# Performance work log

Measured on AMD Instinct MI355X. Metric: run time of the kernel, lower is better.

The kernel has to match this reference:

```python
import jax, jax.numpy as jnp
import numpy as np
from jax import lax

NF = 64
RED = 16  # CALayer / CBAM channel reduction


def conv1x1(x, w, b):
    # x: [B,Ci,H,W], w: [Co,Ci], b: [Co]
    return jnp.einsum('oi,bihw->bohw', w, x) + b[None, :, None, None]


def calayer(x, w1, b1, w2, b2):
    # SE-style channel attention (RCAN CALayer): global avg pool -> 1x1 conv -> ReLU -> 1x1 conv -> sigmoid
    y = x.mean(axis=(2, 3))                      # [B,C]
    z = jax.nn.relu(y @ w1.T + b1)               # [B,C//RED]
    s = jax.nn.sigmoid(z @ w2.T + b2)            # [B,C]
    return x * s[:, :, None, None]


def mean_variance_norm(x, eps=1e-5):
    # per-sample, per-channel spatial instance norm (AdaAttN style)
    m = x.mean(axis=(2, 3), keepdims=True)
    v = x.var(axis=(2, 3), keepdims=True)
    return (x - m) / jnp.sqrt(v + eps)


def cbam(x, mlp_w1, mlp_b1, mlp_w2, mlp_b2, sp_w, sp_b):
    # BasicAttentionBlockv1 assumed to be a CBAM block (docstring: "CBAM")
    avg = x.mean(axis=(2, 3))                    # [B,C]
    mx = x.max(axis=(2, 3))                      # [B,C]
    def mlp(v):
        return jax.nn.relu(v @ mlp_w1.T + mlp_b1) @ mlp_w2.T + mlp_b2
    s = jax.nn.sigmoid(mlp(avg) + mlp(mx))       # [B,C]
    x = x * s[:, :, None, None]
    sp_in = jnp.concatenate([x.mean(axis=1, keepdims=True), x.max(axis=1, keepdims=True)], axis=1)  # [B,2,H,W]
    m = lax.conv_general_dilated(sp_in, sp_w, (1, 1), 'SAME',
                                 dimension_numbers=('NCHW', 'OIHW', 'NCHW')) + sp_b[None, :, None, None]
    return x * jax.nn.sigmoid(m)


def setup_inputs() -> dict:
    key = jax.random.key(0)
    ks = iter(jax.random.split(key, 64))
    B, N, C, H, W = 4, 3, NF, 64, 64
    r = lambda shape, s=0.05: jax.random.normal(next(ks), shape, dtype=jnp.float32) * s
    inp = {
        'group': jax.random.normal(next(ks), (B, N, C, H, W), dtype=jnp.float32),
        'FG': jax.random.normal(next(ks), (B, N, C, H, W), dtype=jnp.float32),
        'BG': jax.random.normal(next(ks), (B, N, C, H, W), dtype=jnp.float32),
        # conv_group_1 (3nf->3nf 1x1), CALayer(3nf), conv_group_2 (3nf->nf), conv_group_3 (nf->nf)
        'wg1': r((3 * C, 3 * C)), 'bg1': r((3 * C,)),
        'cag_w1': r((3 * C // RED, 3 * C)), 'cag_b1': r((3 * C // RED,)),
        'cag_w2': r((3 * C, 3 * C // RED)), 'cag_b2': r((3 * C,)),
        'wg2': r((C, 3 * C)), 'bg2': r((C,)),
        'wg3': r((C, C)), 'bg3': r((C,)),
        # conv_center_1, CALayer(nf), conv_center_2
        'wc1': r((C, C)), 'bc1': r((C,)),
        'cac_w1': r((C // RED, C)), 'cac_b1': r((C // RED,)),
        'cac_w2': r((C, C // RED)), 'cac_b2': r((C,)),
        'wc2': r((C, C)), 'bc2': r((C,)),
        # f, g, h 1x1 convs
        'f_w': r((C, C)), 'f_b': r((C,)),
        'g_w': r((C, C)), 'g_b': r((C,)),
        'h_w': r((C, C)), 'h_b': r((C,)),
        # CBAM params
        'mlp_w1': r((C // RED, C)), 'mlp_b1': r((C // RED,)),
        'mlp_w2': r((C, C // RED)), 'mlp_b2': r((C,)),
        'sp_w': r((1, 2, 7, 7)), 'sp_b': r((1,)),
    }
    return inp


def reference(group, FG, BG,
              wg1, bg1, cag_w1, cag_b1, cag_w2, cag_b2, wg2, bg2, wg3, bg3,
              wc1, bc1, cac_w1, cac_b1, cac_w2, cac_b2, wc2, bc2,
              f_w, f_b, g_w, g_b, h_w, h_b,
              mlp_w1, mlp_b1, mlp_w2, mlp_b2, sp_w, sp_b):
    B, N, C, H, W = group.shape
    center = group[:, 1]
    FGc = FG[:, 1]
    BGc = BG[:, 1]
    grp = group.reshape(B, N * C, H, W)

    fea_group = conv1x1(grp, wg1, bg1)
    fea_group = calayer(fea_group, cag_w1, cag_b1, cag_w2, cag_b2)
    fea_group = conv1x1(fea_group, wg2, bg2)
    fea_group = conv1x1(fea_group, wg3, bg3)

    fea_center = conv1x1(center, wc1, bc1)
    fea_center = calayer(fea_center, cac_w1, cac_b1, cac_w2, cac_b2)
    fea_center = conv1x1(fea_center, wc2, bc2)

    Fq = conv1x1(fea_group, f_w, f_b).reshape(B, C, H * W).transpose(0, 2, 1)   # [B,HW,C]
    Gk = conv1x1(fea_center, g_w, g_b).reshape(B, C, H * W)                     # [B,C,HW]
    Hv = conv1x1(BGc, h_w, h_b).reshape(B, C, H * W).transpose(0, 2, 1)         # [B,HW,C]

    S = jax.nn.softmax(jnp.einsum('bqc,bck->bqk', Fq, Gk), axis=-1)             # [B,HW,HW]
    mean = jnp.einsum('bqk,bkc->bqc', S, Hv)                                    # [B,HW,C]
    second = jnp.einsum('bqk,bkc->bqc', S, Hv * Hv)
    std = jnp.sqrt(jax.nn.relu(second - mean * mean))

    mean = mean.reshape(B, H, W, C).transpose(0, 3, 1, 2)
    std = std.reshape(B, H, W, C).transpose(0, 3, 1, 2)

    transfer_FG = std * mean_variance_norm(FGc) + mean
    out = cbam(transfer_FG + BGc, mlp_w1, mlp_b1, mlp_w2, mlp_b2, sp_w, sp_b)
    return out
```

## Files before the change

kernel.cpp:

```cpp
#include <hip/hip_runtime.h>
#include <hip/hip_bf16.h>
#include <math.h>

#define HW 4096

typedef __attribute__((ext_vector_type(8))) short bf16x8;
typedef __attribute__((ext_vector_type(4))) float f32x4;

static __device__ __forceinline__ unsigned short f2bf(float x) {
    unsigned u = __float_as_uint(x);
    u += 0x7fffu + ((u >> 16) & 1u);
    return (unsigned short)(u >> 16);
}
static __device__ __forceinline__ float bf2f(unsigned short h) {
    return __uint_as_float((unsigned)h << 16);
}
static __device__ __forceinline__ float g4(const float4& v, int k) {
    return k == 0 ? v.x : k == 1 ? v.y : k == 2 ? v.z : v.w;
}

__global__ __launch_bounds__(256) void k_transpose2(
    const float* __restrict__ group, const float* __restrict__ BGc, int bstride,
    unsigned short* __restrict__ X0T, unsigned short* __restrict__ BGcT)
{
    extern __shared__ float lds[];
    const int b = blockIdx.y, p0 = blockIdx.x << 6, t = threadIdx.x;
    const int z = blockIdx.z;
    const int C = z ? 64 : 192;
    const float* xb = (z ? BGc : group) + (size_t)b * bstride;
    unsigned short* outT = z ? BGcT : X0T;
    for (int idx = t; idx < (C << 6); idx += 256) {
        int c = idx >> 6, p = idx & 63;
        lds[c * 65 + p] = xb[(size_t)c * HW + p0 + p];
    }
    __syncthreads();
    unsigned short* ob = outT + ((size_t)b * HW + p0) * C;
    for (int idx = t; idx < (C << 6); idx += 256) {
        int p = idx / C, c = idx - p * C;
        ob[idx] = f2bf(lds[c * 65 + p]);
    }
}

__global__ __launch_bounds__(256) void k_xmean(
    const float* __restrict__ g, int bstride, float* __restrict__ xmean)
{
    int bc = blockIdx.x;
    int b = bc / 192, ci = bc - b * 192;
    const float* p = g + (size_t)b * bstride + (size_t)ci * HW;
    int t = threadIdx.x;
    float s = 0.f;
    #pragma unroll 4
    for (int i = t; i < HW; i += 256) s += p[i];
    for (int o = 32; o > 0; o >>= 1) s += __shfl_down(s, o, 64);
    __shared__ float red[4];
    if ((t & 63) == 0) red[t >> 6] = s;
    __syncthreads();
    if (t == 0) xmean[bc] = (red[0] + red[1] + red[2] + red[3]) * (1.0f / HW);
}

static __device__ __forceinline__ void gemm64_tile(
    const float* A, const float* B, int t, float acc[4][4])
{
    const int tr = t >> 4, tc = t & 15;
    #pragma unroll
    for (int i = 0; i < 4; ++i)
        #pragma unroll
        for (int j = 0; j < 4; ++j) acc[i][j] = 0.f;
    for (int k4 = 0; k4 < 64; k4 += 4) {
        float4 a[4], bb[4];
        #pragma unroll
        for (int i = 0; i < 4; ++i) a[i]  = *(const float4*)&A[(4 * tr + i) * 68 + k4];
        #pragma unroll
        for (int kk = 0; kk < 4; ++kk) bb[kk] = *(const float4*)&B[(k4 + kk) * 68 + 4 * tc];
        #pragma unroll
        for (int i = 0; i < 4; ++i)
            #pragma unroll
            for (int kk = 0; kk < 4; ++kk)
                #pragma unroll
                for (int j = 0; j < 4; ++j)
                    acc[i][j] = fmaf(g4(a[i], kk), g4(bb[kk], j), acc[i][j]);
    }
}

__global__ __launch_bounds__(256) void k_prep(
    const float* __restrict__ xmean,
    const float* __restrict__ wg1, const float* __restrict__ bg1,
    const float* __restrict__ cag_w1, const float* __restrict__ cag_b1,
    const float* __restrict__ cag_w2, const float* __restrict__ cag_b2,
    const float* __restrict__ wc1, const float* __restrict__ bc1,
    const float* __restrict__ cac_w1, const float* __restrict__ cac_b1,
    const float* __restrict__ cac_w2, const float* __restrict__ cac_b2,
    const float* __restrict__ wg2, const float* __restrict__ bg2,
    const float* __restrict__ wg3, const float* __restrict__ bg3,
    const float* __restrict__ wc2, const float* __restrict__ bc2,
    const float* __restrict__ wf, const float* __restrict__ fb,
    const float* __restrict__ wgw, const float* __restrict__ gbv,
    const float* __restrict__ wh,
    float* __restrict__ W3L, float* __restrict__ Uf,
    float* __restrict__ bQ0L, float* __restrict__ bK0,
    float* __restrict__ sgG, float* __restrict__ scG,
    unsigned short* __restrict__ whb, unsigned short* __restrict__ wg1b)
{
    const float LOG2E = 1.4426950408889634f;
    __shared__ float sA[64 * 68], sB[64 * 68], sC[64 * 68];
    __shared__ float xm[192], pg[192], pc[64], zz[16];
    const int bid = blockIdx.x, t = threadIdx.x;

    if (bid >= 4) {
        const int x = bid - 4;
        #pragma unroll
        for (int j = 0; j < 16; ++j) {
            int idx = t + j * 256, r = idx >> 6, c = idx & 63;
            sA[r * 68 + c] = wf[idx];
            sB[r * 68 + c] = wg3[idx];
        }
        __syncthreads();
        float acc[4][4];
        gemm64_tile(sA, sB, t, acc);
        {
            const int tr = t >> 4, tc = t & 15;
            #pragma unroll
            for (int i = 0; i < 4; ++i)
                #pragma unroll
                for (int j = 0; j < 4; ++j)
                    sC[(4 * tr + i) * 68 + 4 * tc + j] = acc[i][j];
        }
        __syncthreads();
        if (x == 0 && t < 64) {
            float a = fb[t];
            #pragma unroll 16
            for (int m = 0; m < 64; ++m) {
                a = fmaf(sC[t * 68 + m], bg2[m], a);
                a = fmaf(sA[t * 68 + m], bg3[m], a);
            }
            bQ0L[t] = a * LOG2E;
        }
        __syncthreads();
        for (int idx = t; idx < 3072; idx += 256) {
            int c = idx >> 6, m = idx & 63;
            sA[c * 68 + m] = wg2[m * 192 + x * 48 + c];
        }
        __syncthreads();
        {
            const int tr = t >> 4, tc = t & 15;
            float a2[4][3];
            #pragma unroll
            for (int i = 0; i < 4; ++i)
                #pragma unroll
                for (int j = 0; j < 3; ++j) a2[i][j] = 0.f;
            for (int k4 = 0; k4 < 64; k4 += 4) {
                float4 a[4], bb[3];
                #pragma unroll
                for (int i = 0; i < 4; ++i) a[i] = *(const float4*)&sC[(4 * tr + i) * 68 + k4];
                #pragma unroll
                for (int j = 0; j < 3; ++j) bb[j] = *(const float4*)&sA[(3 * tc + j) * 68 + k4];
                #pragma unroll
                for (int i = 0; i < 4; ++i)
                    #pragma unroll
                    for (int j = 0; j < 3; ++j)
                        #pragma unroll
                        for (int kk = 0; kk < 4; ++kk)
                            a2[i][j] = fmaf(g4(a[i], kk), g4(bb[j], kk), a2[i][j]);
            }
            #pragma unroll
            for (int i = 0; i < 4; ++i)
                #pragma unroll
                for (int j = 0; j < 3; ++j)
                    W3L[(4 * tr + i) * 192 + x * 48 + 3 * tc + j] = a2[i][j] * LOG2E;
        }
        if (x == 1) {
            __syncthreads();
            #pragma unroll
            for (int j = 0; j < 16; ++j) {
                int idx = t + j * 256, r = idx >> 6, c = idx & 63;
                sA[r * 68 + c] = wgw[idx];
                sB[r * 68 + c] = wc2[idx];
            }
            __syncthreads();
            float au[4][4];
            gemm64_tile(sA, sB, t, au);
            {
                const int tr = t >> 4, tc = t & 15;
                #pragma unroll
                for (int i = 0; i < 4; ++i)
                    #pragma unroll
                    for (int j = 0; j < 4; ++j)
                        Uf[(4 * tr + i) * 64 + 4 * tc + j] = au[i][j];
            }
            if (t < 64) {
                float a = gbv[t];
                #pragma unroll 16
                for (int m = 0; m < 64; ++m) a = fmaf(sA[t * 68 + m], bc2[m], a);
                bK0[t] = a;
            }
        }
        for (int idx = t; idx < 9216; idx += 256) {
            int g = x * 9216 + idx;
            wg1b[g] = f2bf(wg1[g]);
        }
        return;
    }

    const int b = bid, w = t >> 6, lane = t & 63;
    if (t < 192) xm[t] = xmean[b * 192 + t];
    __syncthreads();
    for (int r = w; r < 192; r += 4) {
        float part = 0.f;
        #pragma unroll
        for (int j = 0; j < 3; ++j)
            part = fmaf(wg1[r * 192 + lane + 64 * j], xm[lane + 64 * j], part);
        #pragma unroll
        for (int o = 32; o > 0; o >>= 1) part += __shfl_down(part, o, 64);
        if (lane == 0) pg[r] = part + bg1[r];
    }
    for (int r = w; r < 64; r += 4) {
        float part = wc1[r * 64 + lane] * xm[64 + lane];
        #pragma unroll
        for (int o = 32; o > 0; o >>= 1) part += __shfl_down(part, o, 64);
        if (lane == 0) pc[r] = part + bc1[r];
    }
    __syncthreads();
    if (t < 12) {
        float a = cag_b1[t];
        #pragma unroll 16
        for (int i = 0; i < 192; ++i) a = fmaf(cag_w1[t * 192 + i], pg[i], a);
        zz[t] = fmaxf(a, 0.f);
    }
    if (t >= 64 && t < 68) {
        int r = t - 64;
        float a = cac_b1[r];
        #pragma unroll 16
        for (int i = 0; i < 64; ++i) a = fmaf(cac_w1[r * 64 + i], pc[i], a);
        zz[12 + r] = fmaxf(a, 0.f);
    }
    __syncthreads();
    if (t < 192) {
        float a = cag_b2[t];
        #pragma unroll
        for (int j = 0; j < 12; ++j) a = fmaf(cag_w2[t * 12 + j], zz[j], a);
        sgG[b * 192 + t] = 1.f / (1.f + __expf(-a));
    } else {
        int c = t - 192;
        float a = cac_b2[c];
        #pragma unroll
        for (int j = 0; j < 4; ++j) a = fmaf(cac_w2[c * 4 + j], zz[12 + j], a);
        scG[b * 64 + c] = 1.f / (1.f + __expf(-a));
    }
    if (b == 0) {
        #pragma unroll
        for (int j = 0; j < 16; ++j) whb[t + j * 256] = f2bf(wh[t + j * 256]);
    }
}

__global__ __launch_bounds__(256) void k_wscale(
    const float* __restrict__ W3L, const float* __restrict__ Uf,
    const float* __restrict__ sgG, const float* __restrict__ scG,
    const float* __restrict__ wc1, const float* __restrict__ bc1,
    const float* __restrict__ bK0,
    unsigned short* __restrict__ WQs, unsigned short* __restrict__ WKb,
    float* __restrict__ biasK)
{
    const int bid = blockIdx.x, t = threadIdx.x;
    if (bid < 192) {
        int i = bid * 256 + t;
        int b = i / 12288, rem = i - b * 12288;
        int c = rem % 192;
        WQs[i] = f2bf(W3L[rem] * sgG[b * 192 + c]);
        return;
    }
    __shared__ float Usc[64 * 68], sW[64 * 68], u2[64];
    const int b = bid - 192;
    #pragma unroll
    for (int j = 0; j < 16; ++j) {
        int idx = t + j * 256, r = idx >> 6, c = idx & 63;
        Usc[r * 68 + c] = Uf[idx] * scG[b * 64 + c];
        sW[r * 68 + c]  = wc1[idx];
    }
    if (t < 64) u2[t] = scG[b * 64 + t] * bc1[t];
    __syncthreads();
    float acc[4][4];
    gemm64_tile(Usc, sW, t, acc);
    const int tr = t >> 4, tc = t & 15;
    #pragma unroll
    for (int i = 0; i < 4; ++i)
        #pragma unroll
        for (int j = 0; j < 4; ++j)
            WKb[(size_t)b * 4096 + (4 * tr + i) * 64 + 4 * tc + j] = f2bf(acc[i][j]);
    if (t < 64) {
        float a = bK0[t];
        #pragma unroll 16
        for (int m = 0; m < 64; ++m) a = fmaf(Uf[t * 64 + m], u2[m], a);
        biasK[b * 64 + t] = a;
    }
}

__global__ __launch_bounds__(256) void k_gconv(
    const unsigned short* __restrict__ X0T, const unsigned short* __restrict__ wg1b,
    const float* __restrict__ bg1, unsigned short* __restrict__ g1T)
{
    const int t = threadIdx.x;
    const int w = t >> 6, lane = t & 63;
    const int gid = lane >> 4, cid = lane & 15;
    const int b = blockIdx.z;
    const int p0 = blockIdx.x << 6;
    const int co16 = ((blockIdx.y << 2) + w) << 4;
    const unsigned short* xrow = X0T + (size_t)b * HW * 192;
    const unsigned short* wr = wg1b + (size_t)co16 * 192;
    f32x4 acc[4];
    #pragma unroll
    for (int n = 0; n < 4; ++n)
        #pragma unroll
        for (int r = 0; r < 4; ++r)
            acc[n][r] = bg1[co16 + 4 * gid + r];
    for (int kc = 0; kc < 192; kc += 32) {
        bf16x8 a = *(const bf16x8*)(wr + (size_t)cid * 192 + kc + 8 * gid);
        #pragma unroll
        for (int n = 0; n < 4; ++n) {
            bf16x8 bfr = *(const bf16x8*)(xrow + (size_t)(p0 + 16 * n + cid) * 192 + kc + 8 * gid);
            acc[n] = __builtin_amdgcn_mfma_f32_16x16x32_bf16(a, bfr, acc[n], 0, 0, 0);
        }
    }
    #pragma unroll
    for (int n = 0; n < 4; ++n)
        #pragma unroll
        for (int r = 0; r < 4; ++r)
            g1T[((size_t)b * HW + p0 + 16 * n + cid) * 192 + co16 + 4 * gid + r] = f2bf(acc[n][r]);
}

__global__ __launch_bounds__(256) void k_proj(
    const unsigned short* __restrict__ g1T, const unsigned short* __restrict__ X0T,
    const unsigned short* __restrict__ BGcT,
    const unsigned short* __restrict__ WQs, const float* __restrict__ bQ0L,
    const unsigned short* __restrict__ WKb, const float* __restrict__ biasK,
    const unsigned short* __restrict__ whb, const float* __restrict__ h_b,
    unsigned short* __restrict__ FqT, unsigned short* __restrict__ GkT,
    unsigned short* __restrict__ hvN)
{
    const int t = threadIdx.x;
    const int w = t >> 6, lane = t & 63;
    const int gid = lane >> 4, cid = lane & 15;
    const int which = blockIdx.y;
    const int b = blockIdx.z;
    const int p0 = blockIdx.x << 6;
    const int co16 = w << 4;
    int Cin, kOff, ldx;
    const unsigned short *XT, *W;
    const float* bp;
    if (which == 0)      { XT = g1T;  ldx = 192; kOff = 0;  Cin = 192; W = WQs + (size_t)b * 12288; bp = bQ0L; }
    else if (which == 1) { XT = X0T;  ldx = 192; kOff = 64; Cin = 64;  W = WKb + (size_t)b * 4096;  bp = biasK + b * 64; }
    else                 { XT = BGcT; ldx = 64;  kOff = 0;  Cin = 64;  W = whb;                      bp = h_b; }
    const unsigned short* xrow = XT + (size_t)b * HW * ldx + kOff;
    const unsigned short* wr = W + (size_t)co16 * Cin;
    f32x4 acc[4];
    #pragma unroll
    for (int n = 0; n < 4; ++n)
        #pragma unroll
        for (int r = 0; r < 4; ++r)
            acc[n][r] = bp[co16 + 4 * gid + r];
    for (int kc = 0; kc < Cin; kc += 32) {
        bf16x8 a = *(const bf16x8*)(wr + (size_t)cid * Cin + kc + 8 * gid);
        #pragma unroll
        for (int n = 0; n < 4; ++n) {
            bf16x8 bfr = *(const bf16x8*)(xrow + (size_t)(p0 + 16 * n + cid) * ldx + kc + 8 * gid);
            acc[n] = __builtin_amdgcn_mfma_f32_16x16x32_bf16(a, bfr, acc[n], 0, 0, 0);
        }
    }
    #pragma unroll
    for (int n = 0; n < 4; ++n)
        #pragma unroll
        for (int r = 0; r < 4; ++r) {
            float v = acc[n][r];
            int co = co16 + 4 * gid + r;
            int p  = p0 + 16 * n + cid;
            if (which == 0)      FqT[((size_t)b * HW + p) * 64 + co] = f2bf(v);
            else if (which == 1) GkT[((size_t)b * HW + p) * 64 + co] = f2bf(v);
            else                 hvN[((size_t)b * 64 + co) * HW + p] = f2bf(v);
        }
}

__global__ __launch_bounds__(512, 2) void k_attn(
    const unsigned short* __restrict__ FqT, const unsigned short* __restrict__ GkT,
    const unsigned short* __restrict__ HvN,
    float* __restrict__ mb, float* __restrict__ sbuf)
{
    __shared__ __align__(16) char smem[65536];
    const int t = threadIdx.x;
    const int bid = blockIdx.x;
    const int b = (bid & 7) >> 1;
    const int qbase = (((bid >> 3) << 1) | (bid & 1)) << 6;
    const int w = t >> 6, lane = t & 63;
    const int gid = lane >> 4, cid = lane & 15;
    const size_t CQ = (size_t)HW * 64;
    const unsigned short* fqt = FqT + (size_t)b * CQ;
    const unsigned short* gkt = GkT + (size_t)b * CQ;
    const unsigned short* hv  = HvN + (size_t)b * CQ;
    unsigned short* Pw = (unsigned short*)smem + w * 4096;

    bf16x8 fqa[4][2];
    #pragma unroll
    for (int qt = 0; qt < 4; ++qt) {
        const unsigned short* fr = fqt + (size_t)(qbase + 16 * qt + cid) * 64 + 8 * gid;
        fqa[qt][0] = *(const bf16x8*)fr;
        fqa[qt][1] = *(const bf16x8*)(fr + 32);
    }
    bf16x8 ones;
    #pragma unroll
    for (int j = 0; j < 8; ++j) ones[j] = (short)0x3F80;

    const f32x4 fz = {0.f, 0.f, 0.f, 0.f};
    f32x4 am[4][4], a2[4][4], lac[4];
    #pragma unroll
    for (int qt = 0; qt < 4; ++qt) {
        lac[qt] = fz;
        #pragma unroll
        for (int n = 0; n < 4; ++n) { am[qt][n] = fz; a2[qt][n] = fz; }
    }

    const int k00 = w << 9;
    for (int it = 0; it < 8; ++it) {
        const int k0 = k00 + (it << 6);
        #pragma unroll
        for (int n = 0; n < 4; ++n) {
            const unsigned short* gr = gkt + (size_t)(k0 + 16 * n + cid) * 64 + 8 * gid;
            bf16x8 b0 = *(const bf16x8*)gr;
            bf16x8 b1 = *(const bf16x8*)(gr + 32);
            const int k = 16 * n + cid;
            #pragma unroll
            for (int qt = 0; qt < 4; ++qt) {
                f32x4 s = __builtin_amdgcn_mfma_f32_16x16x32_bf16(fqa[qt][0], b0, fz, 0, 0, 0);
                s = __builtin_amdgcn_mfma_f32_16x16x32_bf16(fqa[qt][1], b1, s, 0, 0, 0);
                #pragma unroll
                for (int r = 0; r < 4; ++r) {
                    int q = 4 * gid + r;
                    Pw[qt * 1024 + q * 64 + (((k >> 3) ^ (q & 7)) << 3) + (k & 7)] =
                        f2bf(__builtin_amdgcn_exp2f(s[r]));
                }
            }
        }
        bf16x8 pa[4][2];
        #pragma unroll
        for (int qt = 0; qt < 4; ++qt)
            #pragma unroll
            for (int kh = 0; kh < 2; ++kh)
                pa[qt][kh] = *(const bf16x8*)(Pw + qt * 1024 + cid * 64 +
                                              (((4 * kh + gid) ^ (cid & 7)) << 3));
        #pragma unroll
        for (int qt = 0; qt < 4; ++qt) {
            lac[qt] = __builtin_amdgcn_mfma_f32_16x16x32_bf16(pa[qt][0], ones, lac[qt], 0, 0, 0);
            lac[qt] = __builtin_amdgcn_mfma_f32_16x16x32_bf16(pa[qt][1], ones, lac[qt], 0, 0, 0);
        }
        #pragma unroll
        for (int n = 0; n < 4; ++n) {
            const unsigned short* hr = hv + (size_t)(16 * n + cid) * HW + k0;
            #pragma unroll
            for (int kh = 0; kh < 2; ++kh) {
                bf16x8 hb = *(const bf16x8*)(hr + 32 * kh + 8 * gid);
                bf16x8 h2;
                #pragma unroll
                for (int j = 0; j < 8; ++j) {
                    float v = bf2f((unsigned short)hb[j]);
                    h2[j] = (short)f2bf(v * v);
                }
                #pragma unroll
                for (int qt = 0; qt < 4; ++qt) {
                    am[qt][n] = __builtin_amdgcn_mfma_f32_16x16x32_bf16(pa[qt][kh], hb, am[qt][n], 0, 0, 0);
                    a2[qt][n] = __builtin_amdgcn_mfma_f32_16x16x32_bf16(pa[qt][kh], h2, a2[qt][n], 0, 0, 0);
                }
            }
        }
    }

    __syncthreads();
    float* lb = (float*)smem;
    #pragma unroll
    for (int qt = 0; qt < 4; ++qt)
        *(f32x4*)(lb + ((size_t)(w * 4 + qt) * 64 + lane) * 4) = lac[qt];
    __syncthreads();
    float* Lm = (float*)(smem + 32768);
    if (t < 256) {
        int qt = t >> 6, ls = t & 63;
        f32x4 s = fz;
        #pragma unroll
        for (int ww = 0; ww < 8; ++ww)
            s += *(const f32x4*)(lb + ((size_t)(ww * 4 + qt) * 64 + ls) * 4);
        *(f32x4*)(Lm + ((size_t)qt * 64 + ls) * 4) = s;
    }
    __syncthreads();
    float* ab = (float*)smem;
    f32x4 meanv = fz;
    for (int qt = 0; qt < 4; ++qt) {
        #pragma unroll
        for (int n = 0; n < 4; ++n)
            *(f32x4*)(ab + ((size_t)(w * 4 + n) * 64 + lane) * 4) = am[qt][n];
        __syncthreads();
        if (t < 256) {
            int n = t >> 6, ls = t & 63;
            f32x4 s = fz;
            #pragma unroll
            for (int ww = 0; ww < 8; ++ww)
                s += *(const f32x4*)(ab + ((size_t)(ww * 4 + n) * 64 + ls) * 4);
            f32x4 lv = *(const f32x4*)(Lm + ((size_t)qt * 64 + ls) * 4);
            #pragma unroll
            for (int r = 0; r < 4; ++r) meanv[r] = s[r] / lv[r];
            int q0s = qbase + 16 * qt + 4 * (ls >> 4);
            int c   = 16 * n + (ls & 15);
            *(f32x4*)(mb + (size_t)b * CQ + (size_t)c * HW + q0s) = meanv;
        }
        __syncthreads();
        #pragma unroll
        for (int n = 0; n < 4; ++n)
            *(f32x4*)(ab + ((size_t)(w * 4 + n) * 64 + lane) * 4) = a2[qt][n];
        __syncthreads();
        if (t < 256) {
            int n = t >> 6, ls = t & 63;
            f32x4 s = fz;
            #pragma unroll
            for (int ww = 0; ww < 8; ++ww)
                s += *(const f32x4*)(ab + ((size_t)(ww * 4 + n) * 64 + ls) * 4);
            f32x4 lv = *(const f32x4*)(Lm + ((size_t)qt * 64 + ls) * 4);
            f32x4 sv;
            #pragma unroll
            for (int r = 0; r < 4; ++r) {
                float sec = s[r] / lv[r];
                sv[r] = sqrtf(fmaxf(sec - meanv[r] * meanv[r], 0.f));
            }
            int q0s = qbase + 16 * qt + 4 * (ls >> 4);
            int c   = 16 * n + (ls & 15);
            *(f32x4*)(sbuf + (size_t)b * CQ + (size_t)c * HW + q0s) = sv;
        }
        __syncthreads();
    }
}

__global__ __launch_bounds__(256) void k_transfer_f(
    const float* __restrict__ mb, const float* __restrict__ sb,
    const float* __restrict__ FG, const float* __restrict__ BG, int bstride,
    float* __restrict__ xb, float* __restrict__ pavg, float* __restrict__ pmaxb)
{
    __shared__ float fgl[4096];
    __shared__ float r1[4], r2[4];
    const int bc = blockIdx.x, t = threadIdx.x;
    const int b = bc >> 6, c = bc & 63;
    const size_t row = (size_t)bc * HW;
    const float* fg = FG + (size_t)b * bstride + (size_t)(64 + c) * HW;
    const float* bg = BG + (size_t)b * bstride + (size_t)(64 + c) * HW;
    float s = 0.f, s2 = 0.f;
    #pragma unroll
    for (int j = 0; j < 16; ++j) {
        int i = t + j * 256;
        float v = fg[i];
        fgl[i] = v;
        s += v; s2 += v * v;
    }
    #pragma unroll
    for (int o = 32; o > 0; o >>= 1) { s += __shfl_down(s, o, 64); s2 += __shfl_down(s2, o, 64); }
    if ((t & 63) == 0) { r1[t >> 6] = s; r2[t >> 6] = s2; }
    __syncthreads();
    float m  = (r1[0] + r1[1] + r1[2] + r1[3]) * (1.0f / HW);
    float e2 = (r2[0] + r2[1] + r2[2] + r2[3]) * (1.0f / HW);
    float rs = rsqrtf(fmaxf(e2 - m * m, 0.f) + 1e-5f);
    float psum = 0.f, pmax = -1e30f;
    #pragma unroll
    for (int j = 0; j < 16; ++j) {
        int q = t + j * 256;
        float xv = sb[row + q] * (fgl[q] - m) * rs + mb[row + q] + bg[q];
        xb[row + q] = xv;
        psum += xv; pmax = fmaxf(pmax, xv);
    }
    __syncthreads();
    #pragma unroll
    for (int o = 32; o > 0; o >>= 1) {
        psum += __shfl_down(psum, o, 64);
        pmax = fmaxf(pmax, __shfl_down(pmax, o, 64));
    }
    if ((t & 63) == 0) { r1[t >> 6] = psum; r2[t >> 6] = pmax; }
    __syncthreads();
    if (t == 0) {
        pavg[bc]  = (r1[0] + r1[1] + r1[2] + r1[3]) * (1.0f / HW);
        pmaxb[bc] = fmaxf(fmaxf(r2[0], r2[1]), fmaxf(r2[2], r2[3]));
    }
}

static __device__ __forceinline__ void cbam_scale(
    const float* __restrict__ pav, const float* __restrict__ pmx,
    const float* __restrict__ w1, const float* __restrict__ b1,
    const float* __restrict__ w2, const float* __restrict__ b2,
    int b, int t, float* scb)
{
    __shared__ float za[4], zm[4];
    if (t < 4) {
        float aa = b1[t], am = b1[t];
        #pragma unroll 16
        for (int i = 0; i < 64; ++i) {
            aa = fmaf(w1[t * 64 + i], pav[b * 64 + i], aa);
            am = fmaf(w1[t * 64 + i], pmx[b * 64 + i], am);
        }
        za[t] = fmaxf(aa, 0.f);
        zm[t] = fmaxf(am, 0.f);
    }
    __syncthreads();
    if (t < 64) {
        float a = 2.f * b2[t];
        #pragma unroll
        for (int j = 0; j < 4; ++j) a = fmaf(w2[t * 4 + j], za[j] + zm[j], a);
        scb[t] = 1.f / (1.f + __expf(-a));
    }
    __syncthreads();
}

__global__ __launch_bounds__(256) void k_sp_pool(
    const float* __restrict__ xb,
    const float* __restrict__ pav, const float* __restrict__ pmx,
    const float* __restrict__ w1, const float* __restrict__ b1,
    const float* __restrict__ w2, const float* __restrict__ b2,
    float* __restrict__ spm, float* __restrict__ spx)
{
    __shared__ float scb[64];
    const int b = blockIdx.y, t = threadIdx.x;
    cbam_scale(pav, pmx, w1, b1, w2, b2, b, t, scb);
    const int p = blockIdx.x * 256 + t;
    const float* xp = xb + (size_t)b * 262144 + p;
    float sum = 0.f, mx = -1e30f;
    #pragma unroll 8
    for (int c = 0; c < 64; ++c) {
        float v = xp[(size_t)c * HW] * scb[c];
        sum += v;
        mx = fmaxf(mx, v);
    }
    spm[b * HW + p] = sum * (1.0f / 64.0f);
    spx[b * HW + p] = mx;
}

__global__ __launch_bounds__(256) void k_spf(
    const float* __restrict__ spm, const float* __restrict__ spx,
    const float* __restrict__ w, const float* __restrict__ bias,
    const float* __restrict__ xb,
    const float* __restrict__ pav, const float* __restrict__ pmx,
    const float* __restrict__ w1, const float* __restrict__ b1,
    const float* __restrict__ w2, const float* __restrict__ b2,
    float* __restrict__ out)
{
    __shared__ float scb[64];
    const int b = blockIdx.y, t = threadIdx.x;
    cbam_scale(pav, pmx, w1, b1, w2, b2, b, t, scb);
    const int p = blockIdx.x * 256 + t;
    const int y = p >> 6, x = p & 63;
    float acc = bias[0];
    for (int dy = 0; dy < 7; ++dy) {
        int yy = y + dy - 3;
        if (yy < 0 || yy >= 64) continue;
        for (int dx = 0; dx < 7; ++dx) {
            int xx = x + dx - 3;
            if (xx < 0 || xx >= 64) continue;
            int q = b * HW + yy * 64 + xx;
            acc = fmaf(spm[q], w[dy * 7 + dx],      acc);
            acc = fmaf(spx[q], w[49 + dy * 7 + dx], acc);
        }
    }
    float sgm = 1.f / (1.f + __expf(-acc));
    const float* xp = xb + (size_t)b * 262144 + p;
    float* op = out + (size_t)b * 262144 + p;
    #pragma unroll 8
    for (int c = 0; c < 64; ++c)
        op[(size_t)c * HW] = xp[(size_t)c * HW] * scb[c] * sgm;
}

extern "C" void kernel_launch(void* const* d_in, const int* in_sizes, int n_in,
                              void* d_out, int out_size, void* d_ws, size_t ws_size,
                              hipStream_t stream)
{
    const float* group  = (const float*)d_in[0];
    const float* FG     = (const float*)d_in[1];
    const float* BG     = (const float*)d_in[2];
    const float* wg1    = (const float*)d_in[3];
    const float* bg1    = (const float*)d_in[4];
    const float* cag_w1 = (const float*)d_in[5];
    const float* cag_b1 = (const float*)d_in[6];
    const float* cag_w2 = (const float*)d_in[7];
    const float* cag_b2 = (const float*)d_in[8];
    const float* wg2    = (const float*)d_in[9];
    const float* bg2    = (const float*)d_in[10];
    const float* wg3    = (const float*)d_in[11];
    const float* bg3    = (const float*)d_in[12];
    const float* wc1    = (const float*)d_in[13];
    const float* bc1    = (const float*)d_in[14];
    const float* cac_w1 = (const float*)d_in[15];
    const float* cac_b1 = (const float*)d_in[16];
    const float* cac_w2 = (const float*)d_in[17];
    const float* cac_b2 = (const float*)d_in[18];
    const float* wc2    = (const float*)d_in[19];
    const float* bc2    = (const float*)d_in[20];
    const float* f_w    = (const float*)d_in[21];
    const float* f_b    = (const float*)d_in[22];
    const float* g_w    = (const float*)d_in[23];
    const float* g_b    = (const float*)d_in[24];
    const float* h_w    = (const float*)d_in[25];
    const float* h_b    = (const float*)d_in[26];
    const float* mlp_w1 = (const float*)d_in[27];
    const float* mlp_b1 = (const float*)d_in[28];
    const float* mlp_w2 = (const float*)d_in[29];
    const float* mlp_b2 = (const float*)d_in[30];
    const float* sp_w   = (const float*)d_in[31];
    const float* sp_b   = (const float*)d_in[32];
    float* out = (float*)d_out;

    const int B = 4;
    const size_t CHW = (size_t)64 * HW;
    const int BST = (int)(3 * CHW);

    float* ws = (float*)d_ws;
    const size_t M = 1048576;
    unsigned short* X0T  = (unsigned short*)ws;
    unsigned short* BGcT = (unsigned short*)(ws + 3 * M / 2);
    unsigned short* g1T  = (unsigned short*)(ws + 2 * M);
    unsigned short* FqT  = (unsigned short*)(ws + 7 * M / 2);
    unsigned short* GkT  = (unsigned short*)(ws + 4 * M);
    unsigned short* hvN  = (unsigned short*)(ws + 9 * M / 2);
    float* mbuf = ws + 5 * M;
    float* sbuf = ws + 6 * M;
    float* xb   = ws;
    float* smalls = ws + 7 * M;
    float* xmean = smalls;
    float* sgG   = smalls + 768;
    float* scG   = smalls + 1536;
    float* pav   = smalls + 1792;
    float* pmx   = smalls + 2048;
    float* biasK = smalls + 2304;
    float* bQ0L  = smalls + 2560;
    float* bK0   = smalls + 2624;
    float* Uf    = smalls + 2688;
    float* W3L   = smalls + 6784;
    float* spm   = smalls + 19072;
    float* spx   = smalls + 35456;
    unsigned short* wsh = (unsigned short*)(smalls + 51840);
    unsigned short* WQs  = wsh;
    unsigned short* WKb  = wsh + 49152;
    unsigned short* whb  = wsh + 65536;
    unsigned short* wg1b = wsh + 69632;

    dim3 blk(256);

    k_transpose2<<<dim3(64, B, 2), blk, 192 * 65 * 4, stream>>>(group, BG + CHW, BST, X0T, BGcT);
    k_xmean<<<B * 192, blk, 0, stream>>>(group, BST, xmean);
    k_prep<<<8, blk, 0, stream>>>(
        xmean, wg1, bg1, cag_w1, cag_b1, cag_w2, cag_b2,
        wc1, bc1, cac_w1, cac_b1, cac_w2, cac_b2,
        wg2, bg2, wg3, bg3, wc2, bc2,
        f_w, f_b, g_w, g_b, h_w,
        W3L, Uf, bQ0L, bK0, sgG, scG, whb, wg1b);
    k_wscale<<<196, blk, 0, stream>>>(W3L, Uf, sgG, scG, wc1, bc1, bK0, WQs, WKb, biasK);
    k_gconv<<<dim3(64, 3, B), blk, 0, stream>>>(X0T, wg1b, bg1, g1T);
    k_proj<<<dim3(64, 3, B), blk, 0, stream>>>(
        g1T, X0T, BGcT, WQs, bQ0L, WKb, biasK, whb, h_b, FqT, GkT, hvN);
    k_attn<<<256, 512, 0, stream>>>(FqT, GkT, hvN, mbuf, sbuf);
    k_transfer_f<<<B * 64, blk, 0, stream>>>(mbuf, sbuf, FG, BG, BST, xb, pav, pmx);
    k_sp_pool<<<dim3(HW / 256, B), blk, 0, stream>>>(xb, pav, pmx, mlp_w1, mlp_b1, mlp_w2, mlp_b2, spm, spx);
    k_spf<<<dim3(HW / 256, B), blk, 0, stream>>>(spm, spx, sp_w, sp_b, xb, pav, pmx, mlp_w1, mlp_b1, mlp_w2, mlp_b2, out);
}
```

Measured before the change: 164.5 us.

## Fuse xmean into transpose, precompute Hv squared, use packed bf16 convert

Folds the per-channel mean of the group input into the transpose kernel via wave reductions and atomics, so the separate xmean pass that re-read the input is gone (a memset is added instead). Hv*Hv is computed once in the projection kernel and stored as its own bf16 tensor, so the attention kernel no longer squares and rounds it in every block. That costs an extra global read stream in attention. Exp results are converted with the packed v_cvt_pk_bf16_f32 instruction instead of manual rounding. The workspace layout is rearranged to fit the new buffer.

Measured after the change: 203.8 us. +23.9%, slower.

```diff
diff --git a/kernel.cpp b/kernel.cpp
--- a/kernel.cpp
+++ b/kernel.cpp
@@ -12,8 +12,10 @@
     u += 0x7fffu + ((u >> 16) & 1u);
     return (unsigned short)(u >> 16);
 }
-static __device__ __forceinline__ float bf2f(unsigned short h) {
-    return __uint_as_float((unsigned)h << 16);
+static __device__ __forceinline__ unsigned cvtpk(float a, float b) {
+    unsigned d;
+    asm("v_cvt_pk_bf16_f32 %0, %1, %2" : "=v"(d) : "v"(a), "v"(b));
+    return d;
 }
 static __device__ __forceinline__ float g4(const float4& v, int k) {
     return k == 0 ? v.x : k == 1 ? v.y : k == 2 ? v.z : v.w;
@@ -21,7 +23,8 @@
 
 __global__ __launch_bounds__(256) void k_transpose2(
     const float* __restrict__ group, const float* __restrict__ BGc, int bstride,
-    unsigned short* __restrict__ X0T, unsigned short* __restrict__ BGcT)
+    unsigned short* __restrict__ X0T, unsigned short* __restrict__ BGcT,
+    float* __restrict__ xmean)
 {
     extern __shared__ float lds[];
     const int b = blockIdx.y, p0 = blockIdx.x << 6, t = threadIdx.x;
@@ -39,23 +42,15 @@
         int p = idx / C, c = idx - p * C;
         ob[idx] = f2bf(lds[c * 65 + p]);
     }
-}
-
-__global__ __launch_bounds__(256) void k_xmean(
-    const float* __restrict__ g, int bstride, float* __restrict__ xmean)
-{
-    int bc = blockIdx.x;
-    int b = bc / 192, ci = bc - b * 192;
-    const float* p = g + (size_t)b * bstride + (size_t)ci * HW;
-    int t = threadIdx.x;
-    float s = 0.f;
-    #pragma unroll 4
-    for (int i = t; i < HW; i += 256) s += p[i];
-    for (int o = 32; o > 0; o >>= 1) s += __shfl_down(s, o, 64);
-    __shared__ float red[4];
-    if ((t & 63) == 0) red[t >> 6] = s;
-    __syncthreads();
-    if (t == 0) xmean[bc] = (red[0] + red[1] + red[2] + red[3]) * (1.0f / HW);
+    if (z == 0) {
+        const int w = t >> 6, lane = t & 63;
+        for (int c = w; c < 192; c += 4) {
+            float v = lds[c * 65 + lane];
+            #pragma unroll
+            for (int o = 32; o > 0; o >>= 1) v += __shfl_down(v, o, 64);
+            if (lane == 0) atomicAdd(&xmean[b * 192 + c], v * (1.0f / HW));
+        }
+    }
 }
 
 static __device__ __forceinline__ void gemm64_tile(
@@ -334,7 +329,7 @@
     const unsigned short* __restrict__ WKb, const float* __restrict__ biasK,
     const unsigned short* __restrict__ whb, const float* __restrict__ h_b,
     unsigned short* __restrict__ FqT, unsigned short* __restrict__ GkT,
-    unsigned short* __restrict__ hvN)
+    unsigned short* __restrict__ hvN, unsigned short* __restrict__ hv2N)
 {
     const int t = threadIdx.x;
     const int w = t >> 6, lane = t & 63;
@@ -374,13 +369,17 @@
             int p  = p0 + 16 * n + cid;
             if (which == 0)      FqT[((size_t)b * HW + p) * 64 + co] = f2bf(v);
             else if (which == 1) GkT[((size_t)b * HW + p) * 64 + co] = f2bf(v);
-            else                 hvN[((size_t)b * 64 + co) * HW + p] = f2bf(v);
+            else {
+                size_t o = ((size_t)b * 64 + co) * HW + p;
+                hvN[o]  = f2bf(v);
+                hv2N[o] = f2bf(v * v);
+            }
         }
 }
 
 __global__ __launch_bounds__(512, 2) void k_attn(
     const unsigned short* __restrict__ FqT, const unsigned short* __restrict__ GkT,
-    const unsigned short* __restrict__ HvN,
+    const unsigned short* __restrict__ HvN, const unsigned short* __restrict__ Hv2N,
     float* __restrict__ mb, float* __restrict__ sbuf)
 {
     __shared__ __align__(16) char smem[65536];
@@ -394,6 +393,7 @@
     const unsigned short* fqt = FqT + (size_t)b * CQ;
     const unsigned short* gkt = GkT + (size_t)b * CQ;
     const unsigned short* hv  = HvN + (size_t)b * CQ;
+    const unsigned short* hv2 = Hv2N + (size_t)b * CQ;
     unsigned short* Pw = (unsigned short*)smem + w * 4096;
 
     bf16x8 fqa[4][2];
@@ -429,11 +429,15 @@
             for (int qt = 0; qt < 4; ++qt) {
                 f32x4 s = __builtin_amdgcn_mfma_f32_16x16x32_bf16(fqa[qt][0], b0, fz, 0, 0, 0);
                 s = __builtin_amdgcn_mfma_f32_16x16x32_bf16(fqa[qt][1], b1, s, 0, 0, 0);
+                unsigned d0 = cvtpk(__builtin_amdgcn_exp2f(s[0]), __builtin_amdgcn_exp2f(s[1]));
+                unsigned d1 = cvtpk(__builtin_amdgcn_exp2f(s[2]), __builtin_amdgcn_exp2f(s[3]));
+                unsigned short pv[4] = {
+                    (unsigned short)d0, (unsigned short)(d0 >> 16),
+                    (unsigned short)d1, (unsigned short)(d1 >> 16) };
                 #pragma unroll
                 for (int r = 0; r < 4; ++r) {
                     int q = 4 * gid + r;
-                    Pw[qt * 1024 + q * 64 + (((k >> 3) ^ (q & 7)) << 3) + (k & 7)] =
-                        f2bf(__builtin_amdgcn_exp2f(s[r]));
+                    Pw[qt * 1024 + q * 64 + (((k >> 3) ^ (q & 7)) << 3) + (k & 7)] = pv[r];
                 }
             }
         }
@@ -451,16 +455,12 @@
         }
         #pragma unroll
         for (int n = 0; n < 4; ++n) {
-            const unsigned short* hr = hv + (size_t)(16 * n + cid) * HW + k0;
+            const unsigned short* hr  = hv  + (size_t)(16 * n + cid) * HW + k0;
+            const unsigned short* hr2 = hv2 + (size_t)(16 * n + cid) * HW + k0;
             #pragma unroll
             for (int kh = 0; kh < 2; ++kh) {
-                bf16x8 hb = *(const bf16x8*)(hr + 32 * kh + 8 * gid);
-                bf16x8 h2;
-                #pragma unroll
-                for (int j = 0; j < 8; ++j) {
-                    float v = bf2f((unsigned short)hb[j]);
-                    h2[j] = (short)f2bf(v * v);
-                }
+                bf16x8 hb = *(const bf16x8*)(hr  + 32 * kh + 8 * gid);
+                bf16x8 h2 = *(const bf16x8*)(hr2 + 32 * kh + 8 * gid);
                 #pragma unroll
                 for (int qt = 0; qt < 4; ++qt) {
                     am[qt][n] = __builtin_amdgcn_mfma_f32_16x16x32_bf16(pa[qt][kh], hb, am[qt][n], 0, 0, 0);
@@ -716,10 +716,11 @@
     unsigned short* FqT  = (unsigned short*)(ws + 7 * M / 2);
     unsigned short* GkT  = (unsigned short*)(ws + 4 * M);
     unsigned short* hvN  = (unsigned short*)(ws + 9 * M / 2);
-    float* mbuf = ws + 5 * M;
-    float* sbuf = ws + 6 * M;
+    unsigned short* hv2N = (unsigned short*)(ws + 5 * M);
+    float* mbuf = ws + 2 * M;
+    float* sbuf = ws + 11 * M / 2;
     float* xb   = ws;
-    float* smalls = ws + 7 * M;
+    float* smalls = ws + 13 * M / 2;
     float* xmean = smalls;
     float* sgG   = smalls + 768;
     float* scG   = smalls + 1536;
@@ -740,8 +741,8 @@
 
     dim3 blk(256);
 
-    k_transpose2<<<dim3(64, B, 2), blk, 192 * 65 * 4, stream>>>(group, BG + CHW, BST, X0T, BGcT);
-    k_xmean<<<B * 192, blk, 0, stream>>>(group, BST, xmean);
+    hipMemsetAsync(xmean, 0, 768 * sizeof(float), stream);
+    k_transpose2<<<dim3(64, B, 2), blk, 192 * 65 * 4, stream>>>(group, BG + CHW, BST, X0T, BGcT, xmean);
     k_prep<<<8, blk, 0, stream>>>(
         xmean, wg1, bg1, cag_w1, cag_b1, cag_w2, cag_b2,
         wc1, bc1, cac_w1, cac_b1, cac_w2, cac_b2,
@@ -751,8 +752,8 @@
     k_wscale<<<196, blk, 0, stream>>>(W3L, Uf, sgG, scG, wc1, bc1, bK0, WQs, WKb, biasK);
     k_gconv<<<dim3(64, 3, B), blk, 0, stream>>>(X0T, wg1b, bg1, g1T);
     k_proj<<<dim3(64, 3, B), blk, 0, stream>>>(
-        g1T, X0T, BGcT, WQs, bQ0L, WKb, biasK, whb, h_b, FqT, GkT, hvN);
-    k_attn<<<256, 512, 0, stream>>>(FqT, GkT, hvN, mbuf, sbuf);
+        g1T, X0T, BGcT, WQs, bQ0L, WKb, biasK, whb, h_b, FqT, GkT, hvN, hv2N);
+    k_attn<<<256, 512, 0, stream>>>(FqT, GkT, hvN, hv2N, mbuf, sbuf);
     k_transfer_f<<<B * 64, blk, 0, stream>>>(mbuf, sbuf, FG, BG, BST, xb, pav, pmx);
     k_sp_pool<<<dim3(HW / 256, B), blk, 0, stream>>>(xb, pav, pmx, mlp_w1, mlp_b1, mlp_w2, mlp_b2, spm, spx);
     k_spf<<<dim3(HW / 256, B), blk, 0, stream>>>(spm, spx, sp_w, sp_b, xb, pav, pmx, mlp_w1, mlp_b1, mlp_w2, mlp_b2, out);
```

## Fold group conv1x1 into query weights and fuse channel mean into transpose

Applied to the files above, without the earlier changes.

The per-pixel 192x192 group convolution (k_gconv) is replaced by precomputing a combined per-batch weight WQF = WQs·wg1 plus a folded bias in a tiny MFMA kernel, so k_proj reads X0T directly and the g1T intermediate buffer is no longer written and re-read. The separate k_xmean pass over the group tensor is removed; k_transpose2 now writes per-tile channel partial sums from LDS and k_prep reduces them. This saves one full-resolution GEMM, its memory traffic and a kernel launch. In exchange, rounding the composed weight to bf16 changes numerics slightly, and the partial-sum buffer enlarges workspace usage.

New measurement: 170.4 us. +3.6%, slower.

```diff
diff --git a/kernel.cpp b/kernel.cpp
--- a/kernel.cpp
+++ b/kernel.cpp
@@ -21,7 +21,8 @@
 
 __global__ __launch_bounds__(256) void k_transpose2(
     const float* __restrict__ group, const float* __restrict__ BGc, int bstride,
-    unsigned short* __restrict__ X0T, unsigned short* __restrict__ BGcT)
+    unsigned short* __restrict__ X0T, unsigned short* __restrict__ BGcT,
+    float* __restrict__ xpart)
 {
     extern __shared__ float lds[];
     const int b = blockIdx.y, p0 = blockIdx.x << 6, t = threadIdx.x;
@@ -39,23 +40,16 @@
         int p = idx / C, c = idx - p * C;
         ob[idx] = f2bf(lds[c * 65 + p]);
     }
-}
-
-__global__ __launch_bounds__(256) void k_xmean(
-    const float* __restrict__ g, int bstride, float* __restrict__ xmean)
-{
-    int bc = blockIdx.x;
-    int b = bc / 192, ci = bc - b * 192;
-    const float* p = g + (size_t)b * bstride + (size_t)ci * HW;
-    int t = threadIdx.x;
-    float s = 0.f;
-    #pragma unroll 4
-    for (int i = t; i < HW; i += 256) s += p[i];
-    for (int o = 32; o > 0; o >>= 1) s += __shfl_down(s, o, 64);
-    __shared__ float red[4];
-    if ((t & 63) == 0) red[t >> 6] = s;
-    __syncthreads();
-    if (t == 0) xmean[bc] = (red[0] + red[1] + red[2] + red[3]) * (1.0f / HW);
+    if (z == 0) {
+        const int w = t >> 6, lane = t & 63;
+        float* xp = xpart + ((size_t)b * 64 + blockIdx.x) * 192;
+        for (int c = w; c < 192; c += 4) {
+            float v = lds[c * 65 + lane];
+            #pragma unroll
+            for (int o = 32; o > 0; o >>= 1) v += __shfl_down(v, o, 64);
+            if (lane == 0) xp[c] = v;
+        }
+    }
 }
 
 static __device__ __forceinline__ void gemm64_tile(
@@ -83,7 +77,7 @@
 }
 
 __global__ __launch_bounds__(256) void k_prep(
-    const float* __restrict__ xmean,
+    const float* __restrict__ xpart,
     const float* __restrict__ wg1, const float* __restrict__ bg1,
     const float* __restrict__ cag_w1, const float* __restrict__ cag_b1,
     const float* __restrict__ cag_w2, const float* __restrict__ cag_b2,
@@ -99,7 +93,7 @@
     float* __restrict__ W3L, float* __restrict__ Uf,
     float* __restrict__ bQ0L, float* __restrict__ bK0,
     float* __restrict__ sgG, float* __restrict__ scG,
-    unsigned short* __restrict__ whb, unsigned short* __restrict__ wg1b)
+    unsigned short* __restrict__ whb, unsigned short* __restrict__ wg1bT)
 {
     const float LOG2E = 1.4426950408889634f;
     __shared__ float sA[64 * 68], sB[64 * 68], sC[64 * 68];
@@ -195,14 +189,20 @@
             }
         }
         for (int idx = t; idx < 9216; idx += 256) {
-            int g = x * 9216 + idx;
-            wg1b[g] = f2bf(wg1[g]);
+            int ci = x * 48 + idx / 192, mid = idx % 192;
+            wg1bT[(size_t)ci * 192 + mid] = f2bf(wg1[mid * 192 + ci]);
         }
         return;
     }
 
     const int b = bid, w = t >> 6, lane = t & 63;
-    if (t < 192) xm[t] = xmean[b * 192 + t];
+    if (t < 192) {
+        float a = 0.f;
+        #pragma unroll 16
+        for (int pb = 0; pb < 64; ++pb)
+            a += xpart[((size_t)b * 64 + pb) * 192 + t];
+        xm[t] = a * (1.0f / HW);
+    }
     __syncthreads();
     for (int r = w; r < 192; r += 4) {
         float part = 0.f;
@@ -294,43 +294,45 @@
     }
 }
 
-__global__ __launch_bounds__(256) void k_gconv(
-    const unsigned short* __restrict__ X0T, const unsigned short* __restrict__ wg1b,
-    const float* __restrict__ bg1, unsigned short* __restrict__ g1T)
+__global__ __launch_bounds__(256) void k_wqfull(
+    const unsigned short* __restrict__ WQs, const unsigned short* __restrict__ wg1bT,
+    const float* __restrict__ bQ0L, const float* __restrict__ bg1,
+    unsigned short* __restrict__ WQF, float* __restrict__ biasQF)
 {
     const int t = threadIdx.x;
     const int w = t >> 6, lane = t & 63;
     const int gid = lane >> 4, cid = lane & 15;
-    const int b = blockIdx.z;
-    const int p0 = blockIdx.x << 6;
-    const int co16 = ((blockIdx.y << 2) + w) << 4;
-    const unsigned short* xrow = X0T + (size_t)b * HW * 192;
-    const unsigned short* wr = wg1b + (size_t)co16 * 192;
-    f32x4 acc[4];
+    const int xci = blockIdx.x, b = blockIdx.y;
+    const int ci0 = xci << 6, co16 = w << 4;
+    const unsigned short* A = WQs + (size_t)b * 12288 + (size_t)co16 * 192;
+    const f32x4 fz = {0.f, 0.f, 0.f, 0.f};
+    f32x4 acc[4] = {fz, fz, fz, fz};
+    for (int kc = 0; kc < 192; kc += 32) {
+        bf16x8 a = *(const bf16x8*)(A + (size_t)cid * 192 + kc + 8 * gid);
+        #pragma unroll
+        for (int n = 0; n < 4; ++n) {
+            bf16x8 bb = *(const bf16x8*)(wg1bT + (size_t)(ci0 + 16 * n + cid) * 192 + kc + 8 * gid);
+            acc[n] = __builtin_amdgcn_mfma_f32_16x16x32_bf16(a, bb, acc[n], 0, 0, 0);
+        }
+    }
     #pragma unroll
     for (int n = 0; n < 4; ++n)
         #pragma unroll
         for (int r = 0; r < 4; ++r)
-            acc[n][r] = bg1[co16 + 4 * gid + r];
-    for (int kc = 0; kc < 192; kc += 32) {
-        bf16x8 a = *(const bf16x8*)(wr + (size_t)cid * 192 + kc + 8 * gid);
-        #pragma unroll
-        for (int n = 0; n < 4; ++n) {
-            bf16x8 bfr = *(const bf16x8*)(xrow + (size_t)(p0 + 16 * n + cid) * 192 + kc + 8 * gid);
-            acc[n] = __builtin_amdgcn_mfma_f32_16x16x32_bf16(a, bfr, acc[n], 0, 0, 0);
-        }
-    }
-    #pragma unroll
-    for (int n = 0; n < 4; ++n)
-        #pragma unroll
-        for (int r = 0; r < 4; ++r)
-            g1T[((size_t)b * HW + p0 + 16 * n + cid) * 192 + co16 + 4 * gid + r] = f2bf(acc[n][r]);
+            WQF[(size_t)b * 12288 + (size_t)(co16 + 4 * gid + r) * 192 + ci0 + 16 * n + cid] =
+                f2bf(acc[n][r]);
+    if (xci == 0 && t < 64) {
+        float a = bQ0L[t];
+        #pragma unroll 16
+        for (int m = 0; m < 192; ++m)
+            a = fmaf(bf2f(WQs[(size_t)b * 12288 + t * 192 + m]), bg1[m], a);
+        biasQF[b * 64 + t] = a;
+    }
 }
 
 __global__ __launch_bounds__(256) void k_proj(
-    const unsigned short* __restrict__ g1T, const unsigned short* __restrict__ X0T,
-    const unsigned short* __restrict__ BGcT,
-    const unsigned short* __restrict__ WQs, const float* __restrict__ bQ0L,
+    const unsigned short* __restrict__ X0T, const unsigned short* __restrict__ BGcT,
+    const unsigned short* __restrict__ WQF, const float* __restrict__ biasQF,
     const unsigned short* __restrict__ WKb, const float* __restrict__ biasK,
     const unsigned short* __restrict__ whb, const float* __restrict__ h_b,
     unsigned short* __restrict__ FqT, unsigned short* __restrict__ GkT,
@@ -346,7 +348,7 @@
     int Cin, kOff, ldx;
     const unsigned short *XT, *W;
     const float* bp;
-    if (which == 0)      { XT = g1T;  ldx = 192; kOff = 0;  Cin = 192; W = WQs + (size_t)b * 12288; bp = bQ0L; }
+    if (which == 0)      { XT = X0T;  ldx = 192; kOff = 0;  Cin = 192; W = WQF + (size_t)b * 12288; bp = biasQF + b * 64; }
     else if (which == 1) { XT = X0T;  ldx = 192; kOff = 64; Cin = 64;  W = WKb + (size_t)b * 4096;  bp = biasK + b * 64; }
     else                 { XT = BGcT; ldx = 64;  kOff = 0;  Cin = 64;  W = whb;                      bp = h_b; }
     const unsigned short* xrow = XT + (size_t)b * HW * ldx + kOff;
@@ -712,7 +714,6 @@
     const size_t M = 1048576;
     unsigned short* X0T  = (unsigned short*)ws;
     unsigned short* BGcT = (unsigned short*)(ws + 3 * M / 2);
-    unsigned short* g1T  = (unsigned short*)(ws + 2 * M);
     unsigned short* FqT  = (unsigned short*)(ws + 7 * M / 2);
     unsigned short* GkT  = (unsigned short*)(ws + 4 * M);
     unsigned short* hvN  = (unsigned short*)(ws + 9 * M / 2);
@@ -720,38 +721,39 @@
     float* sbuf = ws + 6 * M;
     float* xb   = ws;
     float* smalls = ws + 7 * M;
-    float* xmean = smalls;
-    float* sgG   = smalls + 768;
-    float* scG   = smalls + 1536;
-    float* pav   = smalls + 1792;
-    float* pmx   = smalls + 2048;
-    float* biasK = smalls + 2304;
-    float* bQ0L  = smalls + 2560;
-    float* bK0   = smalls + 2624;
-    float* Uf    = smalls + 2688;
-    float* W3L   = smalls + 6784;
-    float* spm   = smalls + 19072;
-    float* spx   = smalls + 35456;
-    unsigned short* wsh = (unsigned short*)(smalls + 51840);
-    unsigned short* WQs  = wsh;
-    unsigned short* WKb  = wsh + 49152;
-    unsigned short* whb  = wsh + 65536;
-    unsigned short* wg1b = wsh + 69632;
+    float* xpart = smalls;
+    float* sgG   = smalls + 49152;
+    float* scG   = smalls + 49920;
+    float* pav   = smalls + 50176;
+    float* pmx   = smalls + 50432;
+    float* biasK = smalls + 50688;
+    float* bQ0L  = smalls + 50944;
+    float* bK0   = smalls + 51008;
+    float* biasQF= smalls + 51072;
+    float* Uf    = smalls + 51328;
+    float* W3L   = smalls + 55424;
+    float* spm   = smalls + 67712;
+    float* spx   = smalls + 84096;
+    unsigned short* wsh = (unsigned short*)(smalls + 100480);
+    unsigned short* WQs   = wsh;
+    unsigned short* WKb   = wsh + 49152;
+    unsigned short* whb   = wsh + 65536;
+    unsigned short* wg1bT = wsh + 69632;
+    unsigned short* WQF   = wsh + 106496;
 
     dim3 blk(256);
 
-    k_transpose2<<<dim3(64, B, 2), blk, 192 * 65 * 4, stream>>>(group, BG + CHW, BST, X0T, BGcT);
-    k_xmean<<<B * 192, blk, 0, stream>>>(group, BST, xmean);
+    k_transpose2<<<dim3(64, B, 2), blk, 192 * 65 * 4, stream>>>(group, BG + CHW, BST, X0T, BGcT, xpart);
     k_prep<<<8, blk, 0, stream>>>(
-        xmean, wg1, bg1, cag_w1, cag_b1, cag_w2, cag_b2,
+        xpart, wg1, bg1, cag_w1, cag_b1, cag_w2, cag_b2,
         wc1, bc1, cac_w1, cac_b1, cac_w2, cac_b2,
         wg2, bg2, wg3, bg3, wc2, bc2,
         f_w, f_b, g_w, g_b, h_w,
-        W3L, Uf, bQ0L, bK0, sgG, scG, whb, wg1b);
+        W3L, Uf, bQ0L, bK0, sgG, scG, whb, wg1bT);
     k_wscale<<<196, blk, 0, stream>>>(W3L, Uf, sgG, scG, wc1, bc1, bK0, WQs, WKb, biasK);
-    k_gconv<<<dim3(64, 3, B), blk, 0, stream>>>(X0T, wg1b, bg1, g1T);
+    k_wqfull<<<dim3(3, B), blk, 0, stream>>>(WQs, wg1bT, bQ0L, bg1, WQF, biasQF);
     k_proj<<<dim3(64, 3, B), blk, 0, stream>>>(
-        g1T, X0T, BGcT, WQs, bQ0L, WKb, biasK, whb, h_b, FqT, GkT, hvN);
+        X0T, BGcT, WQF, biasQF, WKb, biasK, whb, h_b, FqT, GkT, hvN);
     k_attn<<<256, 512, 0, stream>>>(FqT, GkT, hvN, mbuf, sbuf);
     k_transfer_f<<<B * 64, blk, 0, stream>>>(mbuf, sbuf, FG, BG, BST, xb, pav, pmx);
     k_sp_pool<<<dim3(HW / 256, B), blk, 0, stream>>>(xb, pav, pmx, mlp_w1, mlp_b1, mlp_w2, mlp_b2, spm, spx);
```
